# Kernel tuning notes

Hardware: AMD Instinct MI355X
Metric: run time of the kernel (lower is better)

The kernel has to match this reference:

```python
import jax, jax.numpy as jnp
import numpy as np

B, NQ, NK, DQ, DK, DV, H = 4, 512, 512, 512, 512, 512, 128
NEG_INF = -1e20


def setup_inputs() -> dict:
    key = jax.random.key(0)
    ks = jax.random.split(key, 7)
    Q = jax.random.normal(ks[0], (B, NQ, DQ), dtype=jnp.float32)
    K = jax.random.normal(ks[1], (B, NK, DK), dtype=jnp.float32)
    V = jax.random.normal(ks[2], (B, NK, DV), dtype=jnp.float32)
    # learned params (LazyLinear, bias=False): y = x @ W with W[in, out]
    Wq = jax.random.normal(ks[3], (DQ, H), dtype=jnp.float32) / np.sqrt(DQ)
    Wk = jax.random.normal(ks[4], (DK, H), dtype=jnp.float32) / np.sqrt(DK)
    wv = jax.random.normal(ks[5], (H,), dtype=jnp.float32) / np.sqrt(H)
    valid_lens = jax.random.randint(ks[6], (B,), 1, NK + 1).astype(jnp.int64)
    return {"Q": Q, "K": K, "V": V, "Wq": Wq, "Wk": Wk, "wv": wv,
            "valid_lens": valid_lens}


def reference(Q, K, V, Wq, Wk, wv, valid_lens):
    # Project queries and keys to shared hidden size H
    Qp = Q @ Wq                      # (B, NQ, H)
    Kp = K @ Wk                      # (B, NK, H)
    # Additive (Bahdanau) broadcast: (B, NQ, NK, H)
    S = jnp.tanh(Qp[:, :, None, :] + Kp[:, None, :, :])
    # Linear score to scalar: (B, NQ, NK)
    scores = jnp.einsum('bqkh,h->bqk', S, wv)
    # Mask positions k >= valid_lens[b] (1-D valid_lens broadcast over queries)
    kv_idx = jnp.arange(scores.shape[-1])[None, None, :]
    mask = kv_idx < valid_lens[:, None, None]
    scores = jnp.where(mask, scores, NEG_INF)
    W = jax.nn.softmax(scores, axis=-1)  # dropout rate 0.0 -> identity
    return jnp.einsum('bqk,bkv->bqv', W, V)
```

## Files before the change

kernel.cpp:

```cpp
#include <hip/hip_runtime.h>

#define B_   4
#define NQ_  512
#define NK_  512
#define D_   512
#define H_   128

typedef __attribute__((ext_vector_type(8))) short short8;
typedef __attribute__((ext_vector_type(4))) float f32x4;

__device__ __forceinline__ float fexp2(float x) { return __builtin_amdgcn_exp2f(x); }
__device__ __forceinline__ float frcp(float x)  { return __builtin_amdgcn_rcpf(x); }
__device__ __forceinline__ unsigned short f2bf(float f) {
    unsigned int u = __builtin_bit_cast(unsigned int, f);
    u += 0x7FFFu + ((u >> 16) & 1u);
    return (unsigned short)(u >> 16);
}


#define WS_EQK   0
#define WS_PP    524288
#define WS_WP    4718592
#define WS_WBF   4718848
#define WS_VT    5243136

__global__ __launch_bounds__(256) void prep_kernel(
    const float* __restrict__ Q, const float* __restrict__ K,
    const float* __restrict__ Wq, const float* __restrict__ Wk,
    const float* __restrict__ V,
    float* __restrict__ Pp, unsigned short* __restrict__ Vt)
{
    __shared__ float smem[2 * 32 * 132];
    const int t = threadIdx.x;

    if (blockIdx.x < 32) {
        const int xb = blockIdx.x;
        const int ks = blockIdx.y;
        const bool isQ = xb < 16;
        const float* __restrict__ X = isQ ? Q : K;
        const float* __restrict__ W = isQ ? Wq : Wk;
        const int r0 = (xb & 15) * 128;
        const int k0 = ks * 64;

        float (*At)[132] = (float(*)[132])smem;
        float (*Wl)[132] = (float(*)[132])(smem + 32 * 132);

        const int cg = t & 15;
        const int rg = t >> 4;
        float acc[8][8] = {};

        for (int kc = 0; kc < 2; ++kc) {
            if (kc) __syncthreads();
            #pragma unroll
            for (int p = 0; p < 4; ++p) {
                const int idx = p * 256 + t;
                const int row = idx & 127;
                const int kq  = (idx >> 7) * 4;
                const float4 v = *reinterpret_cast<const float4*>(
                    X + (size_t)(r0 + row) * D_ + k0 + kc * 32 + kq);
                At[kq + 0][row] = v.x; At[kq + 1][row] = v.y;
                At[kq + 2][row] = v.z; At[kq + 3][row] = v.w;
            }
            #pragma unroll
            for (int p = 0; p < 4; ++p) {
                const int idx = p * 256 + t;
                const int kr  = idx >> 5;
                const int c4  = (idx & 31) * 4;
                *reinterpret_cast<float4*>(&Wl[kr][c4]) =
                    *reinterpret_cast<const float4*>(
                        W + (size_t)(k0 + kc * 32 + kr) * H_ + c4);
            }
            __syncthreads();

            #pragma unroll 4
            for (int k = 0; k < 32; ++k) {
                const float4 a0 = *reinterpret_cast<const float4*>(&At[k][rg * 8]);
                const float4 a1 = *reinterpret_cast<const float4*>(&At[k][rg * 8 + 4]);
                const float4 b0 = *reinterpret_cast<const float4*>(&Wl[k][cg * 4]);
                const float4 b1 = *reinterpret_cast<const float4*>(&Wl[k][64 + cg * 4]);
                const float aa[8] = {a0.x, a0.y, a0.z, a0.w, a1.x, a1.y, a1.z, a1.w};
                const float bb[8] = {b0.x, b0.y, b0.z, b0.w, b1.x, b1.y, b1.z, b1.w};
                #pragma unroll
                for (int r = 0; r < 8; ++r)
                    #pragma unroll
                    for (int c = 0; c < 8; ++c)
                        acc[r][c] = fmaf(aa[r], bb[c], acc[r][c]);
            }
        }

        float* __restrict__ dst = Pp + (size_t)blockIdx.y * (4096 * 128);
        #pragma unroll
        for (int r = 0; r < 8; ++r) {
            const int grow = xb * 128 + rg * 8 + r;
            *reinterpret_cast<float4*>(dst + (size_t)grow * H_ + cg * 4) =
                make_float4(acc[r][0], acc[r][1], acc[r][2], acc[r][3]);
            *reinterpret_cast<float4*>(dst + (size_t)grow * H_ + 64 + cg * 4) =
                make_float4(acc[r][4], acc[r][5], acc[r][6], acc[r][7]);
        }
    } else {
        const int id = (blockIdx.x - 32) * 8 + blockIdx.y;
        const int kt = id & 7, dt = (id >> 3) & 7, b = id >> 6;
        float (*Vl)[69] = (float(*)[69])smem;

        #pragma unroll
        for (int p = 0; p < 4; ++p) {
            const int idx = p * 256 + t;
            const int r  = idx >> 4;
            const int c4 = (idx & 15) * 4;
            const float4 v = *reinterpret_cast<const float4*>(
                V + ((size_t)b * NK_ + kt * 64 + r) * D_ + dt * 64 + c4);
            Vl[r][c4 + 0] = v.x; Vl[r][c4 + 1] = v.y;
            Vl[r][c4 + 2] = v.z; Vl[r][c4 + 3] = v.w;
        }
        __syncthreads();

        #pragma unroll
        for (int p = 0; p < 4; ++p) {
            const int idx = p * 256 + t;
            const int d  = idx >> 4;
            const int k4 = (idx & 15) * 4;
            ushort4 o;
            o.x = f2bf(Vl[k4 + 0][d]); o.y = f2bf(Vl[k4 + 1][d]);
            o.z = f2bf(Vl[k4 + 2][d]); o.w = f2bf(Vl[k4 + 3][d]);
            *reinterpret_cast<ushort4*>(
                Vt + ((size_t)b * D_ + dt * 64 + d) * NK_ + kt * 64 + k4) = o;
        }
    }
}

__global__ __launch_bounds__(256) void proj_add_kernel(
    const float* __restrict__ Pp, const float* __restrict__ wv,
    float* __restrict__ Eqk, float* __restrict__ wp)
{
    const int i = blockIdx.x * 256 + threadIdx.x;
    const float C2 = 2.88539008177792681472f;
    float4 s = make_float4(0.f, 0.f, 0.f, 0.f);
    #pragma unroll
    for (int p = 0; p < 8; ++p) {
        const float4 v = reinterpret_cast<const float4*>(Pp)[(size_t)p * 131072 + i];
        s.x += v.x; s.y += v.y; s.z += v.z; s.w += v.w;
    }
    s.x = fexp2(C2 * s.x); s.y = fexp2(C2 * s.y);
    s.z = fexp2(C2 * s.z); s.w = fexp2(C2 * s.w);
    reinterpret_cast<float4*>(Eqk)[i] = s;

    if (blockIdx.x == 0 && threadIdx.x < 64) {
        const float2 w2 = reinterpret_cast<const float2*>(wv)[threadIdx.x];
        const float wn0 = -2.0f * w2.x;
        const float wn1 = -2.0f * w2.y;
        reinterpret_cast<float4*>(wp)[threadIdx.x] =
            make_float4(wn0, wn1, wn0 + wn1, 0.0f);
    }
}

__global__ __launch_bounds__(512, 4) void score_softmax_kernel(
    const float* __restrict__ Eqk, const float* __restrict__ wp,
    const int* __restrict__ valid_lens, unsigned short* __restrict__ Wbf)
{
    const int rb   = blockIdx.x;
    const int t    = threadIdx.x;
    const int w    = __builtin_amdgcn_readfirstlane(t >> 6);
    const int lane = t & 63;
    const int rloc = w >> 1;
    const int half = w & 1;
    const int row  = rb * 4 + rloc;
    const int b    = row >> 9;

    __shared__ __align__(16) float4 Ks[2 * 64 * 33];
    __shared__ float redM[4][2], redS[4][2];

    const float4* __restrict__ Q4 =
        reinterpret_cast<const float4*>(Eqk + (size_t)row * H_);
    const float4* __restrict__ wp4 = reinterpret_cast<const float4*>(wp);
    const float4* __restrict__ Kp4 =
        reinterpret_cast<const float4*>(Eqk + (size_t)(2048 + b * NK_) * H_);

    float vals[4];

    for (int c = 0; c < 4; ++c) {
        if (c) __syncthreads();
        #pragma unroll
        for (int p = 0; p < 8; ++p) {
            const int idx = p * 512 + t;
            const int hh  = idx >> 11;
            const int r   = (idx >> 5) & 63;
            const int h4  = idx & 31;
            Ks[(hh * 64 + r) * 33 + h4] =
                Kp4[(size_t)(hh * 256 + c * 64 + r) * 32 + h4];
        }
        __syncthreads();

        float s = 0.0f;
        #pragma unroll 4
        for (int g = 0; g < 32; ++g) {
            const float4 kv = Ks[(half * 64 + lane) * 33 + g];
            const float4 qa = Q4[g];
            const float4 wa = wp4[2 * g];
            const float4 wb = wp4[2 * g + 1];
            const float e0 = qa.x * kv.x;
            const float e1 = qa.y * kv.y;
            const float e2 = qa.z * kv.z;
            const float e3 = qa.w * kv.w;
            const float D01 = 1.0f + fmaf(e0, e1, e0 + e1);
            const float D23 = 1.0f + fmaf(e2, e3, e2 + e3);
            const float n01 = fmaf(wa.y, e0, fmaf(wa.x, e1, wa.z));
            const float n23 = fmaf(wb.y, e2, fmaf(wb.x, e3, wb.z));
            const float N   = fmaf(n23, D01, n01 * D23);
            s = fmaf(N, frcp(D01 * D23), s);
        }
        vals[c] = s;
    }

    const int vl = valid_lens[b];
    const float L2E = 1.44269504088896340736f;
    float m = -1e30f;
    #pragma unroll
    for (int c = 0; c < 4; ++c) {
        const int k = half * 256 + c * 64 + lane;
        vals[c] = (k < vl) ? vals[c] : -1e30f;
        m = fmaxf(m, vals[c]);
    }
    #pragma unroll
    for (int off = 32; off >= 1; off >>= 1)
        m = fmaxf(m, __shfl_xor(m, off, 64));
    float sum = 0.0f;
    #pragma unroll
    for (int c = 0; c < 4; ++c)
        sum += fexp2((vals[c] - m) * L2E);
    #pragma unroll
    for (int off = 32; off >= 1; off >>= 1)
        sum += __shfl_xor(sum, off, 64);

    if (lane == 0) { redM[rloc][half] = m; redS[rloc][half] = sum; }
    __syncthreads();

    const float m0 = redM[rloc][0], m1 = redM[rloc][1];
    const float s0 = redS[rloc][0], s1 = redS[rloc][1];
    const float M  = fmaxf(m0, m1);
    const float S  = fmaf(s0, fexp2((m0 - M) * L2E),
                          s1 * fexp2((m1 - M) * L2E));
    const float inv = frcp(S);

    unsigned short* __restrict__ dst = Wbf + (size_t)row * NK_ + half * 256;
    #pragma unroll
    for (int c = 0; c < 4; ++c)
        dst[c * 64 + lane] = f2bf(fexp2((vals[c] - M) * L2E) * inv);
}

__global__ __launch_bounds__(256) void av_gemm_kernel(
    const unsigned short* __restrict__ Wbf, const unsigned short* __restrict__ Vt,
    float* __restrict__ O)
{
    const int c0 = blockIdx.x * 64;
    const int r0 = blockIdx.y * 64;
    const int b  = blockIdx.z;
    const int t  = threadIdx.x;
    const int wave = __builtin_amdgcn_readfirstlane(t >> 6);
    const int lane = t & 63;
    const int m    = lane & 15;
    const int quad = lane >> 4;

    __shared__ unsigned short Al [64][136];
    __shared__ unsigned short Btl[64][136];

    f32x4 acc0 = {0.f,0.f,0.f,0.f}, acc1 = {0.f,0.f,0.f,0.f};
    f32x4 acc2 = {0.f,0.f,0.f,0.f}, acc3 = {0.f,0.f,0.f,0.f};

    for (int kc = 0; kc < 4; ++kc) {
        if (kc) __syncthreads();
        #pragma unroll
        for (int p = 0; p < 4; ++p) {
            const int idx = p * 256 + t;
            const int rl = idx >> 4;
            const int k8 = (idx & 15) * 8;
            *reinterpret_cast<uint4*>(&Al[rl][k8]) =
                *reinterpret_cast<const uint4*>(
                    Wbf + ((size_t)b * NQ_ + r0 + rl) * NK_ + kc * 128 + k8);
            *reinterpret_cast<uint4*>(&Btl[rl][k8]) =
                *reinterpret_cast<const uint4*>(
                    Vt + ((size_t)b * D_ + c0 + rl) * NK_ + kc * 128 + k8);
        }
        __syncthreads();

        #pragma unroll
        for (int sub = 0; sub < 4; ++sub) {
            const int kcol = sub * 32 + quad * 8;
            const short8 a = *reinterpret_cast<const short8*>(&Al[wave * 16 + m][kcol]);
            const short8 b0 = *reinterpret_cast<const short8*>(&Btl[ 0 + m][kcol]);
            const short8 b1 = *reinterpret_cast<const short8*>(&Btl[16 + m][kcol]);
            const short8 b2 = *reinterpret_cast<const short8*>(&Btl[32 + m][kcol]);
            const short8 b3 = *reinterpret_cast<const short8*>(&Btl[48 + m][kcol]);
            acc0 = __builtin_amdgcn_mfma_f32_16x16x32_bf16(a, b0, acc0, 0, 0, 0);
            acc1 = __builtin_amdgcn_mfma_f32_16x16x32_bf16(a, b1, acc1, 0, 0, 0);
            acc2 = __builtin_amdgcn_mfma_f32_16x16x32_bf16(a, b2, acc2, 0, 0, 0);
            acc3 = __builtin_amdgcn_mfma_f32_16x16x32_bf16(a, b3, acc3, 0, 0, 0);
        }
    }

    const size_t rowbase = (size_t)b * NQ_ + r0 + wave * 16 + quad * 4;
    #pragma unroll
    for (int i = 0; i < 4; ++i) {
        float* __restrict__ orow = O + (rowbase + i) * D_ + c0 + m;
        orow[ 0] = acc0[i];
        orow[16] = acc1[i];
        orow[32] = acc2[i];
        orow[48] = acc3[i];
    }
}

extern "C" void kernel_launch(void* const* d_in, const int* in_sizes, int n_in,
                              void* d_out, int out_size, void* d_ws, size_t ws_size,
                              hipStream_t stream) {
    (void)in_sizes; (void)n_in; (void)out_size; (void)ws_size;

    const float* Q   = (const float*)d_in[0];
    const float* K   = (const float*)d_in[1];
    const float* V   = (const float*)d_in[2];
    const float* Wq  = (const float*)d_in[3];
    const float* Wk  = (const float*)d_in[4];
    const float* wv  = (const float*)d_in[5];
    const int*   vl  = (const int*)d_in[6];
    float* out = (float*)d_out;

    float* ws  = (float*)d_ws;
    float* Eqk = ws + WS_EQK;
    float* Pp  = ws + WS_PP;
    float* wp  = ws + WS_WP;
    unsigned short* Wbf = (unsigned short*)(ws + WS_WBF);
    unsigned short* Vt  = (unsigned short*)(ws + WS_VT);

    prep_kernel<<<dim3(64, 8), 256, 0, stream>>>(Q, K, Wq, Wk, V, Pp, Vt);
    proj_add_kernel<<<dim3(512), 256, 0, stream>>>(Pp, wv, Eqk, wp);
    score_softmax_kernel<<<dim3(512), 512, 0, stream>>>(Eqk, wp, vl, Wbf);
    av_gemm_kernel<<<dim3(8, 8, 4), 256, 0, stream>>>(Wbf, Vt, out);
}
```

Before: 121.4 us.

## Drop split-K projection partials and fuse reduction and exp into prep kernel

The Q/K projection GEMM no longer splits the K dimension into eight partial buffers that a separate kernel sums and exponentiates. Each block now computes a 32x64 output tile over the full 512-wide reduction and applies the exp2 transform directly, writing Eqk. The wv preprocessing moves into the same kernel. This removes one kernel launch and the write and re-read of the large partial-sum buffer, at the cost of smaller per-thread register tiles (2x4 instead of 8x8) and lower arithmetic intensity per shared-memory load.

```diff
diff --git a/kernel.cpp b/kernel.cpp
--- a/kernel.cpp
+++ b/kernel.cpp
@@ -19,86 +19,94 @@
 
 
 #define WS_EQK   0
-#define WS_PP    524288
-#define WS_WP    4718592
-#define WS_WBF   4718848
-#define WS_VT    5243136
-
-__global__ __launch_bounds__(256) void prep_kernel(
+#define WS_WP    524288
+#define WS_WBF   524544
+#define WS_VT    1048832
+
+__global__ __launch_bounds__(256) void prep2_kernel(
     const float* __restrict__ Q, const float* __restrict__ K,
     const float* __restrict__ Wq, const float* __restrict__ Wk,
-    const float* __restrict__ V,
-    float* __restrict__ Pp, unsigned short* __restrict__ Vt)
+    const float* __restrict__ V, const float* __restrict__ wv,
+    float* __restrict__ Eqk, float* __restrict__ wp,
+    unsigned short* __restrict__ Vt)
 {
-    __shared__ float smem[2 * 32 * 132];
+    __shared__ __align__(16) float smem[64 * 36 + 64 * 68];
     const int t = threadIdx.x;
-
-    if (blockIdx.x < 32) {
-        const int xb = blockIdx.x;
-        const int ks = blockIdx.y;
-        const bool isQ = xb < 16;
+    const float C2 = 2.88539008177792681472f;
+
+    if (blockIdx.x == 0 && t < 64) {
+        const float2 w2 = reinterpret_cast<const float2*>(wv)[t];
+        const float wn0 = -2.0f * w2.x;
+        const float wn1 = -2.0f * w2.y;
+        reinterpret_cast<float4*>(wp)[t] =
+            make_float4(wn0, wn1, wn0 + wn1, 0.0f);
+    }
+
+    if (blockIdx.x < 256) {
+        const int rt = blockIdx.x >> 1;
+        const int ct = blockIdx.x & 1;
+        const int r0 = rt * 32;
+        const bool isQ = r0 < 2048;
         const float* __restrict__ X = isQ ? Q : K;
         const float* __restrict__ W = isQ ? Wq : Wk;
-        const int r0 = (xb & 15) * 128;
-        const int k0 = ks * 64;
-
-        float (*At)[132] = (float(*)[132])smem;
-        float (*Wl)[132] = (float(*)[132])(smem + 32 * 132);
+        const int xr0 = isQ ? r0 : r0 - 2048;
+        const int c0  = ct * 64;
+
+        float (*At)[36] = (float(*)[36])smem;
+        float (*Wl)[68] = (float(*)[68])(smem + 64 * 36);
 
         const int cg = t & 15;
         const int rg = t >> 4;
-        float acc[8][8] = {};
-
-        for (int kc = 0; kc < 2; ++kc) {
+        float acc[2][4] = {};
+
+        for (int kc = 0; kc < 8; ++kc) {
+            const int k0 = kc * 64;
             if (kc) __syncthreads();
             #pragma unroll
-            for (int p = 0; p < 4; ++p) {
+            for (int p = 0; p < 2; ++p) {
                 const int idx = p * 256 + t;
-                const int row = idx & 127;
-                const int kq  = (idx >> 7) * 4;
+                const int row = idx >> 4;
+                const int kq  = (idx & 15) * 4;
                 const float4 v = *reinterpret_cast<const float4*>(
-                    X + (size_t)(r0 + row) * D_ + k0 + kc * 32 + kq);
+                    X + (size_t)(xr0 + row) * D_ + k0 + kq);
                 At[kq + 0][row] = v.x; At[kq + 1][row] = v.y;
                 At[kq + 2][row] = v.z; At[kq + 3][row] = v.w;
             }
             #pragma unroll
             for (int p = 0; p < 4; ++p) {
                 const int idx = p * 256 + t;
-                const int kr  = idx >> 5;
-                const int c4  = (idx & 31) * 4;
+                const int kr  = idx >> 4;
+                const int c4  = (idx & 15) * 4;
                 *reinterpret_cast<float4*>(&Wl[kr][c4]) =
                     *reinterpret_cast<const float4*>(
-                        W + (size_t)(k0 + kc * 32 + kr) * H_ + c4);
+                        W + (size_t)(k0 + kr) * H_ + c0 + c4);
             }
             __syncthreads();
 
-            #pragma unroll 4
-            for (int k = 0; k < 32; ++k) {
-                const float4 a0 = *reinterpret_cast<const float4*>(&At[k][rg * 8]);
-                const float4 a1 = *reinterpret_cast<const float4*>(&At[k][rg * 8 + 4]);
-                const float4 b0 = *reinterpret_cast<const float4*>(&Wl[k][cg * 4]);
-                const float4 b1 = *reinterpret_cast<const float4*>(&Wl[k][64 + cg * 4]);
-                const float aa[8] = {a0.x, a0.y, a0.z, a0.w, a1.x, a1.y, a1.z, a1.w};
-                const float bb[8] = {b0.x, b0.y, b0.z, b0.w, b1.x, b1.y, b1.z, b1.w};
+            #pragma unroll 8
+            for (int k = 0; k < 64; ++k) {
+                const float a0 = At[k][rg * 2];
+                const float a1 = At[k][rg * 2 + 1];
+                const float4 b4 = *reinterpret_cast<const float4*>(&Wl[k][cg * 4]);
+                const float bb[4] = {b4.x, b4.y, b4.z, b4.w};
                 #pragma unroll
-                for (int r = 0; r < 8; ++r)
-                    #pragma unroll
-                    for (int c = 0; c < 8; ++c)
-                        acc[r][c] = fmaf(aa[r], bb[c], acc[r][c]);
+                for (int c = 0; c < 4; ++c) {
+                    acc[0][c] = fmaf(a0, bb[c], acc[0][c]);
+                    acc[1][c] = fmaf(a1, bb[c], acc[1][c]);
+                }
             }
         }
 
-        float* __restrict__ dst = Pp + (size_t)blockIdx.y * (4096 * 128);
-        #pragma unroll
-        for (int r = 0; r < 8; ++r) {
-            const int grow = xb * 128 + rg * 8 + r;
-            *reinterpret_cast<float4*>(dst + (size_t)grow * H_ + cg * 4) =
-                make_float4(acc[r][0], acc[r][1], acc[r][2], acc[r][3]);
-            *reinterpret_cast<float4*>(dst + (size_t)grow * H_ + 64 + cg * 4) =
-                make_float4(acc[r][4], acc[r][5], acc[r][6], acc[r][7]);
+        #pragma unroll
+        for (int r = 0; r < 2; ++r) {
+            float4 o;
+            o.x = fexp2(C2 * acc[r][0]); o.y = fexp2(C2 * acc[r][1]);
+            o.z = fexp2(C2 * acc[r][2]); o.w = fexp2(C2 * acc[r][3]);
+            *reinterpret_cast<float4*>(
+                Eqk + (size_t)(r0 + rg * 2 + r) * H_ + c0 + cg * 4) = o;
         }
     } else {
-        const int id = (blockIdx.x - 32) * 8 + blockIdx.y;
+        const int id = blockIdx.x - 256;
         const int kt = id & 7, dt = (id >> 3) & 7, b = id >> 6;
         float (*Vl)[69] = (float(*)[69])smem;
 
@@ -125,31 +133,6 @@
             *reinterpret_cast<ushort4*>(
                 Vt + ((size_t)b * D_ + dt * 64 + d) * NK_ + kt * 64 + k4) = o;
         }
-    }
-}
-
-__global__ __launch_bounds__(256) void proj_add_kernel(
-    const float* __restrict__ Pp, const float* __restrict__ wv,
-    float* __restrict__ Eqk, float* __restrict__ wp)
-{
-    const int i = blockIdx.x * 256 + threadIdx.x;
-    const float C2 = 2.88539008177792681472f;
-    float4 s = make_float4(0.f, 0.f, 0.f, 0.f);
-    #pragma unroll
-    for (int p = 0; p < 8; ++p) {
-        const float4 v = reinterpret_cast<const float4*>(Pp)[(size_t)p * 131072 + i];
-        s.x += v.x; s.y += v.y; s.z += v.z; s.w += v.w;
-    }
-    s.x = fexp2(C2 * s.x); s.y = fexp2(C2 * s.y);
-    s.z = fexp2(C2 * s.z); s.w = fexp2(C2 * s.w);
-    reinterpret_cast<float4*>(Eqk)[i] = s;
-
-    if (blockIdx.x == 0 && threadIdx.x < 64) {
-        const float2 w2 = reinterpret_cast<const float2*>(wv)[threadIdx.x];
-        const float wn0 = -2.0f * w2.x;
-        const float wn1 = -2.0f * w2.y;
-        reinterpret_cast<float4*>(wp)[threadIdx.x] =
-            make_float4(wn0, wn1, wn0 + wn1, 0.0f);
     }
 }
 
@@ -324,13 +307,11 @@
 
     float* ws  = (float*)d_ws;
     float* Eqk = ws + WS_EQK;
-    float* Pp  = ws + WS_PP;
     float* wp  = ws + WS_WP;
     unsigned short* Wbf = (unsigned short*)(ws + WS_WBF);
     unsigned short* Vt  = (unsigned short*)(ws + WS_VT);
 
-    prep_kernel<<<dim3(64, 8), 256, 0, stream>>>(Q, K, Wq, Wk, V, Pp, Vt);
-    proj_add_kernel<<<dim3(512), 256, 0, stream>>>(Pp, wv, Eqk, wp);
+    prep2_kernel<<<dim3(512), 256, 0, stream>>>(Q, K, Wq, Wk, V, wv, Eqk, wp, Vt);
     score_softmax_kernel<<<dim3(512), 512, 0, stream>>>(Eqk, wp, vl, Wbf);
     av_gemm_kernel<<<dim3(8, 8, 4), 256, 0, stream>>>(Wbf, Vt, out);
 }
```

After: 118.9 us. 2.0% less time.
